# Optimization experiments

Hardware: AMD Instinct MI355X
Metric: run time of the kernel (lower is better)

The kernel has to match this reference:

```python
import jax, jax.numpy as jnp
import numpy as np

IN_C = 64
OUT_C = 64
NUM_RELS = 32
N_NODES = 20000
N_EDGES = 50000


def setup_inputs() -> dict:
    key = jax.random.key(0)
    k1, k2, k3, k4, k5, k6, k7 = jax.random.split(key, 7)
    x = jax.random.normal(k1, (N_NODES, IN_C), dtype=jnp.float32)
    edge_index = jax.random.randint(k2, (2, N_EDGES), 0, N_NODES, dtype=jnp.int64)
    edge_type = jax.random.randint(k3, (N_EDGES,), 0, NUM_RELS, dtype=jnp.int64)
    weight_fwd = jax.random.normal(k4, (NUM_RELS, IN_C * OUT_C), dtype=jnp.float32)
    weight_bwd = jax.random.normal(k5, (NUM_RELS, IN_C * OUT_C), dtype=jnp.float32)
    lin_w = jax.random.normal(k6, (OUT_C, IN_C), dtype=jnp.float32) * (1.0 / np.sqrt(IN_C))
    lin_b = jax.random.normal(k7, (OUT_C,), dtype=jnp.float32) * 0.01
    return {"x": x, "edge_index": edge_index, "edge_type": edge_type,
            "weight_fwd": weight_fwd, "weight_bwd": weight_bwd,
            "lin_w": lin_w, "lin_b": lin_b}


def type_gcn_conv(x, src, dst, edge_type, weight_table):
    # degrees[e] = (# edges sharing src[e]) + 1  (faithful to pairwise-compare count)
    n_nodes = x.shape[0]
    counts = jax.ops.segment_sum(jnp.ones(src.shape[0], jnp.float32), src,
                                 num_segments=n_nodes)
    degrees = counts[src] + 1.0                      # [E]
    w = weight_table[edge_type]                      # [E, in*out] gather
    w = w / (jnp.linalg.norm(w, axis=1, keepdims=True) + 0.01)
    w = w / degrees[:, None]
    w = w.reshape(-1, IN_C, OUT_C)                   # [E, in, out]
    msg = jnp.einsum('ei,eio->eo', x[src], w)        # per-edge small matmul
    return jax.ops.segment_sum(msg, dst, num_segments=n_nodes)  # scatter-add at dst


def reference(x, edge_index, edge_type, weight_fwd, weight_bwd, lin_w, lin_b):
    src, dst = edge_index[0], edge_index[1]
    fwd = type_gcn_conv(x, src, dst, edge_type, weight_fwd)
    # backward conv sees reversed edge_index: its src is original dst
    bwd = type_gcn_conv(x, dst, src, edge_type, weight_bwd)
    return x @ lin_w.T + lin_b + fwd + bwd
```

## Files before the change

kernel.cpp:

```cpp
#include <hip/hip_runtime.h>

#define NREL 32

typedef short short8 __attribute__((ext_vector_type(8)));
typedef float f32x4 __attribute__((ext_vector_type(4)));

__device__ inline unsigned short f2bf(float f) {
    union { float f; unsigned u; } u; u.f = f;
    unsigned r = u.u + 0x7FFF + ((u.u >> 16) & 1);
    return (unsigned short)(r >> 16);
}

__device__ inline void bucket_scan(const int* __restrict__ hist, int lane,
                                   int& h, int& P, int& excl) {
    h = (lane < NREL) ? hist[lane] : 0;
    P = ((h + 63) >> 6) << 6;
    int s = P;
    #pragma unroll
    for (int off = 1; off < 32; off <<= 1) {
        int t = __shfl_up(s, off, 64);
        if ((lane & 31) >= off) s += t;
    }
    excl = s - P;
}


__global__ __launch_bounds__(256) void setup_kernel(
        const float* __restrict__ x,
        const int* __restrict__ src, const int* __restrict__ dst,
        const int* __restrict__ et,
        const float* __restrict__ wf, const float* __restrict__ wb,
        const float* __restrict__ lw, const float* __restrict__ lb,
        float* __restrict__ cntf, float* __restrict__ cntb,
        int* __restrict__ hist, unsigned short* __restrict__ wtb,
        float* __restrict__ out, int E, int N, int nCountB) {
    __shared__ float smem[4 * 8 * 64 + 8];
    int tid = threadIdx.x;
    int b = blockIdx.x;

    if (b < nCountB) {
        int* lh = (int*)smem;
        if (tid < NREL) lh[tid] = 0;
        __syncthreads();
        int e = b * 256 + tid;
        if (e < E) {
            atomicAdd(&cntf[src[e]], 1.0f);
            atomicAdd(&cntb[dst[e]], 1.0f);
            atomicAdd(&lh[et[e]], 1);
        }
        __syncthreads();
        if (tid < NREL && lh[tid]) atomicAdd(&hist[tid], lh[tid]);
        return;
    }
    b -= nCountB;
    if (b < 64) {
        int rel = b & 31, tab = b >> 5;
        const float* s_ = (tab ? wb : wf) + rel * 4096;
        unsigned short* d_ = wtb + (size_t)b * 4096;
        float* part = smem;
        float ssum = 0.f;
        #pragma unroll
        for (int k = 0; k < 16; k += 4) {
            float4 v = *(const float4*)(s_ + tid * 16 + k);
            ssum += v.x * v.x + v.y * v.y + v.z * v.z + v.w * v.w;
        }
        #pragma unroll
        for (int off = 32; off >= 1; off >>= 1) ssum += __shfl_down(ssum, off, 64);
        if ((tid & 63) == 0) part[tid >> 6] = ssum;
        __syncthreads();
        if (tid == 0) part[4] = 1.0f / (sqrtf(part[0] + part[1] + part[2] + part[3]) + 0.01f);
        __syncthreads();
        float sc = part[4];
        int i = tid >> 2, o0 = (tid & 3) * 16;
        #pragma unroll
        for (int q = 0; q < 4; ++q) {
            float4 v = *(const float4*)(s_ + i * 64 + o0 + q * 4);
            d_[(o0 + q * 4 + 0) * 64 + i] = f2bf(v.x * sc);
            d_[(o0 + q * 4 + 1) * 64 + i] = f2bf(v.y * sc);
            d_[(o0 + q * 4 + 2) * 64 + i] = f2bf(v.z * sc);
            d_[(o0 + q * 4 + 3) * 64 + i] = f2bf(v.w * sc);
        }
        return;
    }
    b -= 64;
    {
        int lane = tid & 63, w = tid >> 6;
        int nodeBase = b * 32 + w * 8;
        float4 wrow[16];
        const float4* lwrow = (const float4*)(lw + lane * 64);
        #pragma unroll
        for (int g = 0; g < 16; ++g) wrow[g] = lwrow[g];
        float bias = lb[lane];
        float* xs = smem + w * 8 * 64;
        #pragma unroll
        for (int t = 0; t < 8; ++t) {
            int n = nodeBase + t;
            if (n < N) xs[t * 64 + lane] = x[(size_t)n * 64 + lane];
        }
        __syncthreads();
        for (int t = 0; t < 8; ++t) {
            int n = nodeBase + t;
            if (n >= N) break;
            float acc = bias;
            const float4* xr = (const float4*)(xs + t * 64);
            #pragma unroll
            for (int g = 0; g < 16; ++g) {
                float4 xv = xr[g];
                acc = fmaf(xv.x, wrow[g].x, acc);
                acc = fmaf(xv.y, wrow[g].y, acc);
                acc = fmaf(xv.z, wrow[g].z, acc);
                acc = fmaf(xv.w, wrow[g].w, acc);
            }
            out[(size_t)n * 64 + lane] = acc;
        }
    }
}

__global__ void scatter_kernel(const int* __restrict__ et, int* __restrict__ fill,
                               const int* __restrict__ hist, int* __restrict__ sorted, int E) {
    __shared__ int lh[NREL];
    __shared__ int lbase[NREL];
    __shared__ int bstartS[NREL];
    int tid = threadIdx.x;
    if (tid < 64) {
        int h, P, excl;
        bucket_scan(hist, tid, h, P, excl);
        if (tid < NREL) bstartS[tid] = excl;
    }
    if (tid < NREL) lh[tid] = 0;
    __syncthreads();
    int e = blockIdx.x * blockDim.x + tid;
    int r = 0, my = 0;
    bool valid = (e < E);
    if (valid) { r = et[e]; my = atomicAdd(&lh[r], 1); }
    __syncthreads();
    if (tid < NREL && lh[tid]) lbase[tid] = atomicAdd(&fill[tid], lh[tid]);
    __syncthreads();
    if (valid) sorted[bstartS[r] + lbase[r] + my] = e;
}

#define APITCH 72
__global__ __launch_bounds__(256) void conv_mfma(
        const float* __restrict__ x,
        const int* __restrict__ src, const int* __restrict__ dst,
        const float* __restrict__ cntf, const float* __restrict__ cntb,
        const int* __restrict__ hist,
        const unsigned short* __restrict__ wtb,
        const int* __restrict__ sorted,
        float* __restrict__ out) {
    int tid = threadIdx.x;
    int lane = tid & 63;
    int h, P, excl;
    bucket_scan(hist, lane, h, P, excl);
    int pos = blockIdx.x * 64;
    unsigned long long m_ = __ballot(lane < NREL && pos >= excl && pos < excl + P);
    if (m_ == 0) return;
    int rel = __ffsll(m_) - 1;
    int start = __shfl(excl, rel, 64);
    int hr = __shfl(h, rel, 64);
    int valid = hr - (pos - start);
    if (valid > 64) valid = 64;
    int dir = blockIdx.y;

    __shared__ unsigned short As[64 * APITCH];
    __shared__ unsigned short Bs[64 * APITCH];
    __shared__ int dstS[64];

    int j = tid >> 2, part = tid & 3;

    {
        const uint4* s4 = (const uint4*)(wtb + (size_t)((dir << 5) + rel) * 4096 + j * 64 + part * 16);
        uint4 v0 = s4[0], v1 = s4[1];
        *(uint4*)(&Bs[j * APITCH + part * 16]) = v0;
        *(uint4*)(&Bs[j * APITCH + part * 16 + 8]) = v1;
    }

    if (j >= valid) {
        uint4 z = {0, 0, 0, 0};
        *(uint4*)(&As[j * APITCH + part * 16]) = z;
        *(uint4*)(&As[j * APITCH + part * 16 + 8]) = z;
        if (part == 0) dstS[j] = -1;
    } else {
        int e = sorted[pos + j];
        int s_ = dir ? dst[e] : src[e];
        int d_ = dir ? src[e] : dst[e];
        float cv = dir ? cntb[s_] : cntf[s_];
        float inv = 1.0f / (cv + 1.0f);
        const float4* xr = (const float4*)(x + (size_t)s_ * 64 + part * 16);
        float4 v0 = xr[0], v1 = xr[1], v2 = xr[2], v3 = xr[3];
        uint4 r0, r1;
        r0.x = f2bf(v0.x * inv) | ((unsigned)f2bf(v0.y * inv) << 16);
        r0.y = f2bf(v0.z * inv) | ((unsigned)f2bf(v0.w * inv) << 16);
        r0.z = f2bf(v1.x * inv) | ((unsigned)f2bf(v1.y * inv) << 16);
        r0.w = f2bf(v1.z * inv) | ((unsigned)f2bf(v1.w * inv) << 16);
        r1.x = f2bf(v2.x * inv) | ((unsigned)f2bf(v2.y * inv) << 16);
        r1.y = f2bf(v2.z * inv) | ((unsigned)f2bf(v2.w * inv) << 16);
        r1.z = f2bf(v3.x * inv) | ((unsigned)f2bf(v3.y * inv) << 16);
        r1.w = f2bf(v3.z * inv) | ((unsigned)f2bf(v3.w * inv) << 16);
        *(uint4*)(&As[j * APITCH + part * 16]) = r0;
        *(uint4*)(&As[j * APITCH + part * 16 + 8]) = r1;
        if (part == 0) dstS[j] = d_;
    }
    __syncthreads();

    int w = tid >> 6;
    int m = lane & 15, quad = lane >> 4;
    f32x4 acc0 = {0.f, 0.f, 0.f, 0.f}, acc1 = acc0, acc2 = acc0, acc3 = acc0;
    #pragma unroll
    for (int k0 = 0; k0 < 64; k0 += 32) {
        short8 a  = *(const short8*)(&As[(w * 16 + m) * APITCH + k0 + quad * 8]);
        short8 b0 = *(const short8*)(&Bs[(0  + m) * APITCH + k0 + quad * 8]);
        short8 b1 = *(const short8*)(&Bs[(16 + m) * APITCH + k0 + quad * 8]);
        short8 b2 = *(const short8*)(&Bs[(32 + m) * APITCH + k0 + quad * 8]);
        short8 b3 = *(const short8*)(&Bs[(48 + m) * APITCH + k0 + quad * 8]);
        acc0 = __builtin_amdgcn_mfma_f32_16x16x32_bf16(a, b0, acc0, 0, 0, 0);
        acc1 = __builtin_amdgcn_mfma_f32_16x16x32_bf16(a, b1, acc1, 0, 0, 0);
        acc2 = __builtin_amdgcn_mfma_f32_16x16x32_bf16(a, b2, acc2, 0, 0, 0);
        acc3 = __builtin_amdgcn_mfma_f32_16x16x32_bf16(a, b3, acc3, 0, 0, 0);
    }

    int row_base = w * 16 + quad * 4;
    #pragma unroll
    for (int r = 0; r < 4; ++r) {
        int d_ = dstS[row_base + r];
        if (d_ >= 0) {
            float* op = out + (size_t)d_ * 64 + m;
            atomicAdd(op +  0, acc0[r]);
            atomicAdd(op + 16, acc1[r]);
            atomicAdd(op + 32, acc2[r]);
            atomicAdd(op + 48, acc3[r]);
        }
    }
}

extern "C" void kernel_launch(void* const* d_in, const int* in_sizes, int n_in,
                              void* d_out, int out_size, void* d_ws, size_t ws_size,
                              hipStream_t stream) {
    const float* x  = (const float*)d_in[0];
    const int*   ei = (const int*)  d_in[1];
    const int*   et = (const int*)  d_in[2];
    const float* wf = (const float*)d_in[3];
    const float* wb = (const float*)d_in[4];
    const float* lw = (const float*)d_in[5];
    const float* lb = (const float*)d_in[6];
    float* out = (float*)d_out;

    const int E = in_sizes[2];
    const int N = in_sizes[0] / 64;
    const int maxC = ((E + 63) >> 6) + NREL;

    char* p = (char*)d_ws;
    unsigned short* wtb = (unsigned short*)p;  p += (size_t)2 * NREL * 4096 * sizeof(unsigned short);
    float* cntf = (float*)p;                   p += (size_t)N * sizeof(float);
    float* cntb = (float*)p;                   p += (size_t)N * sizeof(float);
    int*   hist = (int*)p;                     p += NREL * sizeof(int);
    int*   fill = (int*)p;                     p += NREL * sizeof(int);
    int*   sorted = (int*)p;                   p += (size_t)maxC * 64 * sizeof(int);

    const int* srcp = ei;
    const int* dstp = ei + E;

    hipMemsetAsync(cntf, 0, ((size_t)2 * N + 2 * NREL) * sizeof(float), stream);

    const int nCountB = (E + 255) / 256;
    const int nLinB   = (N + 31) / 32;
    setup_kernel<<<nCountB + 64 + nLinB, 256, 0, stream>>>(
        x, srcp, dstp, et, wf, wb, lw, lb, cntf, cntb, hist, wtb, out, E, N, nCountB);
    scatter_kernel<<<(E + 255) / 256, 256, 0, stream>>>(et, fill, hist, sorted, E);
    dim3 cgrid(maxC, 2);
    conv_mfma<<<cgrid, 256, 0, stream>>>(x, srcp, dstp, cntf, cntb, hist, wtb, sorted, out);
}
```

Measured before the change: 115.2 us.

## Pre-convert x to bf16 and pack per-edge src/dst/inv-degree into sorted records

The setup kernel now writes a bf16 copy of x while loading it for the linear layer. The scatter kernel stores a packed int4 record per sorted edge holding src, dst and both inverse degrees, so the conv kernel no longer does an indirect sorted→src/dst→count lookup chain. The conv kernel gathers half-width bf16 rows directly into shared memory and applies the degree scaling after the MFMA, before the atomic adds. This cuts gather bytes and dependent loads, at the cost of extra workspace, an extra bf16 write of x, and a larger scatter kernel.

```diff
diff --git a/kernel.cpp b/kernel.cpp
--- a/kernel.cpp
+++ b/kernel.cpp
@@ -33,6 +33,7 @@
         const float* __restrict__ lw, const float* __restrict__ lb,
         float* __restrict__ cntf, float* __restrict__ cntb,
         int* __restrict__ hist, unsigned short* __restrict__ wtb,
+        unsigned short* __restrict__ xbf,
         float* __restrict__ out, int E, int N, int nCountB) {
     __shared__ float smem[4 * 8 * 64 + 8];
     int tid = threadIdx.x;
@@ -95,7 +96,11 @@
         #pragma unroll
         for (int t = 0; t < 8; ++t) {
             int n = nodeBase + t;
-            if (n < N) xs[t * 64 + lane] = x[(size_t)n * 64 + lane];
+            if (n < N) {
+                float v = x[(size_t)n * 64 + lane];
+                xs[t * 64 + lane] = v;
+                xbf[(size_t)n * 64 + lane] = f2bf(v);
+            }
         }
         __syncthreads();
         for (int t = 0; t < 8; ++t) {
@@ -116,8 +121,11 @@
     }
 }
 
-__global__ void scatter_kernel(const int* __restrict__ et, int* __restrict__ fill,
-                               const int* __restrict__ hist, int* __restrict__ sorted, int E) {
+__global__ void scatter_kernel(const int* __restrict__ src, const int* __restrict__ dst,
+                               const int* __restrict__ et,
+                               const float* __restrict__ cntf, const float* __restrict__ cntb,
+                               int* __restrict__ fill, const int* __restrict__ hist,
+                               int4* __restrict__ einfo, int E) {
     __shared__ int lh[NREL];
     __shared__ int lbase[NREL];
     __shared__ int bstartS[NREL];
@@ -136,17 +144,21 @@
     __syncthreads();
     if (tid < NREL && lh[tid]) lbase[tid] = atomicAdd(&fill[tid], lh[tid]);
     __syncthreads();
-    if (valid) sorted[bstartS[r] + lbase[r] + my] = e;
+    if (valid) {
+        int s = src[e], d = dst[e];
+        float invf = 1.0f / (cntf[s] + 1.0f);
+        float invb = 1.0f / (cntb[d] + 1.0f);
+        einfo[bstartS[r] + lbase[r] + my] =
+            make_int4(s, d, __float_as_int(invf), __float_as_int(invb));
+    }
 }
 
 #define APITCH 72
 __global__ __launch_bounds__(256) void conv_mfma(
-        const float* __restrict__ x,
-        const int* __restrict__ src, const int* __restrict__ dst,
-        const float* __restrict__ cntf, const float* __restrict__ cntb,
+        const unsigned short* __restrict__ xbf,
         const int* __restrict__ hist,
         const unsigned short* __restrict__ wtb,
-        const int* __restrict__ sorted,
+        const int4* __restrict__ einfo,
         float* __restrict__ out) {
     int tid = threadIdx.x;
     int lane = tid & 63;
@@ -165,6 +177,7 @@
     __shared__ unsigned short As[64 * APITCH];
     __shared__ unsigned short Bs[64 * APITCH];
     __shared__ int dstS[64];
+    __shared__ float invS[64];
 
     int j = tid >> 2, part = tid & 3;
 
@@ -179,27 +192,17 @@
         uint4 z = {0, 0, 0, 0};
         *(uint4*)(&As[j * APITCH + part * 16]) = z;
         *(uint4*)(&As[j * APITCH + part * 16 + 8]) = z;
-        if (part == 0) dstS[j] = -1;
+        if (part == 0) { dstS[j] = -1; invS[j] = 0.f; }
     } else {
-        int e = sorted[pos + j];
-        int s_ = dir ? dst[e] : src[e];
-        int d_ = dir ? src[e] : dst[e];
-        float cv = dir ? cntb[s_] : cntf[s_];
-        float inv = 1.0f / (cv + 1.0f);
-        const float4* xr = (const float4*)(x + (size_t)s_ * 64 + part * 16);
-        float4 v0 = xr[0], v1 = xr[1], v2 = xr[2], v3 = xr[3];
-        uint4 r0, r1;
-        r0.x = f2bf(v0.x * inv) | ((unsigned)f2bf(v0.y * inv) << 16);
-        r0.y = f2bf(v0.z * inv) | ((unsigned)f2bf(v0.w * inv) << 16);
-        r0.z = f2bf(v1.x * inv) | ((unsigned)f2bf(v1.y * inv) << 16);
-        r0.w = f2bf(v1.z * inv) | ((unsigned)f2bf(v1.w * inv) << 16);
-        r1.x = f2bf(v2.x * inv) | ((unsigned)f2bf(v2.y * inv) << 16);
-        r1.y = f2bf(v2.z * inv) | ((unsigned)f2bf(v2.w * inv) << 16);
-        r1.z = f2bf(v3.x * inv) | ((unsigned)f2bf(v3.y * inv) << 16);
-        r1.w = f2bf(v3.z * inv) | ((unsigned)f2bf(v3.w * inv) << 16);
-        *(uint4*)(&As[j * APITCH + part * 16]) = r0;
-        *(uint4*)(&As[j * APITCH + part * 16 + 8]) = r1;
-        if (part == 0) dstS[j] = d_;
+        int4 v = einfo[pos + j];
+        int s_ = dir ? v.y : v.x;
+        int d_ = dir ? v.x : v.y;
+        float inv = __int_as_float(dir ? v.w : v.z);
+        const uint4* xr = (const uint4*)(xbf + (size_t)s_ * 64);
+        uint4 a0 = xr[part * 2], a1 = xr[part * 2 + 1];
+        *(uint4*)(&As[j * APITCH + part * 16]) = a0;
+        *(uint4*)(&As[j * APITCH + part * 16 + 8]) = a1;
+        if (part == 0) { dstS[j] = d_; invS[j] = inv; }
     }
     __syncthreads();
 
@@ -222,13 +225,15 @@
     int row_base = w * 16 + quad * 4;
     #pragma unroll
     for (int r = 0; r < 4; ++r) {
-        int d_ = dstS[row_base + r];
+        int row = row_base + r;
+        int d_ = dstS[row];
         if (d_ >= 0) {
+            float inv = invS[row];
             float* op = out + (size_t)d_ * 64 + m;
-            atomicAdd(op +  0, acc0[r]);
-            atomicAdd(op + 16, acc1[r]);
-            atomicAdd(op + 32, acc2[r]);
-            atomicAdd(op + 48, acc3[r]);
+            atomicAdd(op +  0, acc0[r] * inv);
+            atomicAdd(op + 16, acc1[r] * inv);
+            atomicAdd(op + 32, acc2[r] * inv);
+            atomicAdd(op + 48, acc3[r] * inv);
         }
     }
 }
@@ -251,11 +256,12 @@
 
     char* p = (char*)d_ws;
     unsigned short* wtb = (unsigned short*)p;  p += (size_t)2 * NREL * 4096 * sizeof(unsigned short);
+    unsigned short* xbf = (unsigned short*)p;  p += (size_t)N * 64 * sizeof(unsigned short);
     float* cntf = (float*)p;                   p += (size_t)N * sizeof(float);
     float* cntb = (float*)p;                   p += (size_t)N * sizeof(float);
     int*   hist = (int*)p;                     p += NREL * sizeof(int);
     int*   fill = (int*)p;                     p += NREL * sizeof(int);
-    int*   sorted = (int*)p;                   p += (size_t)maxC * 64 * sizeof(int);
+    int4*  einfo = (int4*)p;                   p += (size_t)maxC * 64 * sizeof(int4);
 
     const int* srcp = ei;
     const int* dstp = ei + E;
@@ -265,8 +271,9 @@
     const int nCountB = (E + 255) / 256;
     const int nLinB   = (N + 31) / 32;
     setup_kernel<<<nCountB + 64 + nLinB, 256, 0, stream>>>(
-        x, srcp, dstp, et, wf, wb, lw, lb, cntf, cntb, hist, wtb, out, E, N, nCountB);
-    scatter_kernel<<<(E + 255) / 256, 256, 0, stream>>>(et, fill, hist, sorted, E);
+        x, srcp, dstp, et, wf, wb, lw, lb, cntf, cntb, hist, wtb, xbf, out, E, N, nCountB);
+    scatter_kernel<<<(E + 255) / 256, 256, 0, stream>>>(
+        srcp, dstp, et, cntf, cntb, fill, hist, einfo, E);
     dim3 cgrid(maxC, 2);
-    conv_mfma<<<cgrid, 256, 0, stream>>>(x, srcp, dstp, cntf, cntb, hist, wtb, sorted, out);
-}
+    conv_mfma<<<cgrid, 256, 0, stream>>>(xbf, hist, wtb, einfo, out);
+}
```

Measured after the change: 115.0 us. Within noise of the previous version (-0.2%).
